# Kernel optimization log

Hardware: AMD Instinct MI355X
Metric: run time of the kernel (lower is better)

## Reference

```python
import jax, jax.numpy as jnp
import numpy as np

CHUNK = 128  # single steady-state chunk tier (T divisible by 128)
DECAY_MIN = 0.005


def setup_inputs() -> dict:
    key = jax.random.key(0)
    k0, k1, k2, k3, k4 = jax.random.split(key, 5)
    B, H, T, K = 4, 16, 2048, 64
    r = jax.random.normal(k0, (B, H, T, K), jnp.float32) * 0.5
    k = jax.random.normal(k1, (B, H, T, K), jnp.float32) * 0.5
    v = jax.random.normal(k2, (B, H, T, K), jnp.float32)
    # log-space decay (negative); mild magnitude keeps exp() of cumulative
    # in-chunk decays within fp32 range (torch original upcasts to fp64)
    w = -(jax.random.uniform(k3, (B, H, T, K), jnp.float32) * 0.2 + 0.01)
    u = jax.random.normal(k4, (1, H, 1, K), jnp.float32) * 0.5
    wkv_state = jnp.zeros((B, H, K, K), jnp.float32)
    return {"r": r, "k": k, "v": v, "w": w, "u": u, "wkv_state": wkv_state}


def _chunked_wkv(r, k, v, w, u, wkv_state):
    B, H, T, K = r.shape
    Tc = CHUNK
    N = T // Tc
    # decay preprocessing (log space)
    w_decay = jnp.clip(jnp.exp(w), DECAY_MIN, None)
    w_log = jnp.log(w_decay)
    wc = w_log.reshape(B, H, N, Tc, K)
    wc_cum = jnp.cumsum(wc, axis=-2)                       # inclusive cumsum
    shifted = jnp.pad(wc_cum[..., :-1, :], ((0, 0), (0, 0), (0, 0), (1, 0), (0, 0)))
    ws = wc.sum(axis=-2, keepdims=True)                    # (B,H,N,1,K)
    w_inter = jnp.exp(ws - wc_cum)                          # (B,H,N,Tc,K)
    w_intra = jnp.exp(wc_cum - wc)
    ws_e = jnp.exp(jnp.swapaxes(ws, -1, -2))               # (B,H,N,K,1)

    rc = r.reshape(B, H, N, Tc, K)
    kc = k.reshape(B, H, N, Tc, K)
    vc = v.reshape(B, H, N, Tc, K)

    # numerically-centered intra-chunk decays (offset at chunk midpoint)
    off = shifted[..., Tc // 2:Tc // 2 + 1, :]
    r_dec = jnp.exp(shifted - off)
    k_inv = jnp.exp(off - wc_cum)

    # intra-chunk attention: strictly-lower-triangular + u-bonus diagonal
    a = jnp.einsum('bhnik,bhnjk->bhnij', rc * r_dec, kc * k_inv)
    a = jnp.tril(a, -1)
    diag = jnp.einsum('bhntk,bhntk->bhnt', rc, u[:, :, None] * kc)
    a = a + diag[..., :, None] * jnp.eye(Tc, dtype=a.dtype)
    out = jnp.einsum('bhnij,bhnjv->bhniv', a, vc)

    # inter-chunk: sequential state carry via scan
    wkv = jnp.einsum('bhntk,bhntv->bhnkv', kc * w_inter, vc)   # (B,H,N,K,K)

    def step(state, inp):
        ws_i, wkv_i = inp
        return state * ws_i + wkv_i, state

    ws_s = jnp.moveaxis(ws_e, 2, 0)    # (N,B,H,K,1)
    wkv_s = jnp.moveaxis(wkv, 2, 0)    # (N,B,H,K,K)
    final_state, states = jax.lax.scan(step, wkv_state, (ws_s, wkv_s))
    states = jnp.moveaxis(states, 0, 2)  # (B,H,N,K,K) — state entering chunk n

    out = out + jnp.einsum('bhntk,bhnkv->bhntv', rc * w_intra, states)
    return out.reshape(B, H, T, K), final_state


def reference(r, k, v, w, u, wkv_state):
    return _chunked_wkv(r, k, v, w, u, wkv_state)
```

## Files before the change

### kernel.cpp

```cpp
#include <hip/hip_runtime.h>

#define TC 128
#define KD 64
#define WLOG_MIN (-5.2983174f)

typedef __attribute__((ext_vector_type(8))) short short8;
typedef __attribute__((ext_vector_type(4))) short short4_t;
typedef __attribute__((ext_vector_type(4))) float f32x4;

__device__ __forceinline__ unsigned short f2bf(float x) {
  union { float f; unsigned int u; } c; c.f = x;
  unsigned int u = c.u + 0x7fffu + ((c.u >> 16) & 1u);
  return (unsigned short)(u >> 16);
}
__device__ __forceinline__ float bf2f(unsigned short x) {
  union { unsigned int u; float f; } c; c.u = ((unsigned int)x) << 16; return c.f;
}


__global__ __launch_bounds__(512, 8)
void rwkv_wkv(const float* __restrict__ kk_, const float* __restrict__ vv,
              const float* __restrict__ ww,
              unsigned short* __restrict__ wkv_u16, float* __restrict__ wse_ws,
              int N) {
  __shared__ alignas(16) unsigned short vT_s[KD * TC];
  __shared__ alignas(16) unsigned short kiT_s[KD * TC];
  __shared__ alignas(16) float segtot[8 * 64];

  const int bid = blockIdx.x;
  const int n = bid % N, bh = bid / N;
  const size_t base = ((size_t)bh * N + n) * (TC * KD);
  const float *kg = kk_ + base, *vg = vv + base, *wg = ww + base;

  const int tid = threadIdx.x;
  const int lk = tid & 63;
  const int wv = tid >> 6;

  float wl[16];
  {
    float c = 0.f;
    #pragma unroll
    for (int tt = 0; tt < 16; ++tt) {
      wl[tt] = fmaxf(wg[(wv * 16 + tt) * KD + lk], WLOG_MIN);
      c += wl[tt];
    }
    segtot[wv * 64 + lk] = c;
  }
  __syncthreads();
  float segofs = 0.f, myoff = 0.f, wsum = 0.f;
  #pragma unroll
  for (int i = 0; i < 8; ++i) {
    const float si = segtot[i * 64 + lk];
    if (i < wv) segofs += si;
    if (i < 4) myoff += si;
    wsum += si;
  }
  const float wsoff_own = __expf(wsum - myoff);
  if (wv == 0) wse_ws[((size_t)bh * N + n) * KD + lk] = __expf(wsum);

  {
    float c = segofs;
    short8 vb8, kib8;
    #pragma unroll
    for (int tt = 0; tt < 16; ++tt) {
      const int t = wv * 16 + tt;
      const float kv = kg[t * KD + lk], vvv = vg[t * KD + lk];
      kib8[tt & 7] = (short)f2bf(kv * __expf(myoff - c - wl[tt]));
      vb8[tt & 7] = (short)f2bf(vvv);
      c += wl[tt];
      if ((tt & 7) == 7) {
        const int g = t >> 3;
        *(short8*)&vT_s[lk * TC + ((g ^ (lk & 7)) << 3)] = vb8;
        *(short8*)&kiT_s[lk * TC + ((g ^ (lk & 7)) << 3)] = kib8;
      }
    }
  }
  __syncthreads();

  {
    const int quad = lk >> 4, l16 = lk & 15;
    const int kt = wv >> 1;
    const int nb = (wv & 1) * 2;
    f32x4 acc[2] = {{0,0,0,0},{0,0,0,0}};
    const int row = kt * 16 + l16;
    #pragma unroll
    for (int ks = 0; ks < 4; ++ks) {
      short8 a = *(const short8*)&kiT_s[row * TC + (((ks * 4 + quad) ^ (row & 7)) << 3)];
      #pragma unroll
      for (int nn = 0; nn < 2; ++nn) {
        const int vd = (nb + nn) * 16 + l16;
        short8 b = *(const short8*)&vT_s[vd * TC + (((ks * 4 + quad) ^ (vd & 7)) << 3)];
        acc[nn] = __builtin_amdgcn_mfma_f32_16x16x32_bf16(a, b, acc[nn], 0, 0, 0);
      }
    }
    float wso[4];
    #pragma unroll
    for (int reg = 0; reg < 4; ++reg) wso[reg] = __shfl(wsoff_own, kt * 16 + quad * 4 + reg, 64);
    unsigned short* wkvg = wkv_u16 + ((size_t)bh * N + n) * (KD * KD);
    #pragma unroll
    for (int nn = 0; nn < 2; ++nn)
      #pragma unroll
      for (int reg = 0; reg < 4; ++reg)
        wkvg[(kt * 16 + quad * 4 + reg) * KD + (nb + nn) * 16 + l16] = f2bf(acc[nn][reg] * wso[reg]);
  }
}

__global__ __launch_bounds__(512, 4)
void rwkv_main(const float* __restrict__ rr, const float* __restrict__ kk_,
               const float* __restrict__ vv, const float* __restrict__ ww,
               const float* __restrict__ uu,
               const unsigned short* __restrict__ wkv_u16,
               const float* __restrict__ wse_ws,
               const float* __restrict__ st_in,
               float* __restrict__ out, float* __restrict__ final_out,
               int H, int N) {
  __shared__ alignas(16) unsigned short rd_s[TC * KD];
  __shared__ alignas(16) unsigned short ki_s[TC * KD];
  __shared__ alignas(16) unsigned short vT_s[KD * TC];
  __shared__ alignas(16) unsigned char su_raw[10240];
  __shared__ alignas(16) unsigned short diag_s[TC];
  float* segtot = (float*)su_raw;
  unsigned short* Ast = (unsigned short*)su_raw;

  const int bid = blockIdx.x;
  const int n = bid % N, bh = bid / N, h = bh % H;
  const size_t base = ((size_t)bh * N + n) * (TC * KD);
  const float *rg = rr + base, *kg = kk_ + base, *vg = vv + base, *wg = ww + base;

  const int tid = threadIdx.x;
  const int lk = tid & 63;
  const int wv = tid >> 6;
  const int quad = lk >> 4, l16 = lk & 15;
  const float uk = uu[h * KD + lk];

  float wl[16];
  {
    float c = 0.f;
    #pragma unroll
    for (int tt = 0; tt < 16; ++tt) {
      wl[tt] = fmaxf(wg[(wv * 16 + tt) * KD + lk], WLOG_MIN);
      c += wl[tt];
    }
    segtot[wv * 64 + lk] = c;
  }
  __syncthreads();
  float segofs = 0.f, myoff = 0.f;
  #pragma unroll
  for (int i = 0; i < 8; ++i) {
    const float si = segtot[i * 64 + lk];
    if (i < wv) segofs += si;
    if (i < 4) myoff += si;
  }
  const float eoff = __expf(myoff);

  unsigned int rwp[8];
  {
    float c = segofs;
    short8 vb8;
    float darr[8];
    #pragma unroll
    for (int tt = 0; tt < 16; ++tt) {
      const int t = wv * 16 + tt;
      const float rv = rg[t * KD + lk], kv = kg[t * KD + lk], vvv = vg[t * KD + lk];
      const int slot = (lk >> 3) ^ (t & 7) ^ ((t >> 3) & 7);
      const int nat = t * KD + (slot << 3) + (lk & 7);
      const float e1 = __expf(c - myoff);
      rd_s[nat] = f2bf(rv * e1);
      const unsigned short rwv = f2bf(rv * e1 * eoff);
      if (tt & 1) rwp[tt >> 1] |= ((unsigned int)rwv) << 16;
      else        rwp[tt >> 1]  = (unsigned int)rwv;
      ki_s[nat] = f2bf(kv * __expf(myoff - c - wl[tt]));
      vb8[tt & 7] = (short)f2bf(vvv);
      darr[tt & 7] = rv * uk * kv;
      c += wl[tt];
      if ((tt & 7) == 7) {
        const int g = t >> 3;
        *(short8*)&vT_s[lk * TC + ((g ^ (lk & 7)) << 3)] = vb8;
        #pragma unroll
        for (int o = 32; o > 0; o >>= 1)
          #pragma unroll
          for (int q = 0; q < 8; ++q) darr[q] += __shfl_xor(darr[q], o, 64);
        if (lk == 0) {
          short8 dpk;
          #pragma unroll
          for (int q = 0; q < 8; ++q) dpk[q] = (short)f2bf(darr[q]);
          *(short8*)&diag_s[g * 8] = dpk;
        }
      }
    }
  }
  __syncthreads();

  const int skd = tid >> 3, sv0 = (tid & 7) * 8;
  const size_t sbase = (size_t)bh * (KD * KD);
  float s[8];
  *(f32x4*)&s[0] = *(const f32x4*)&st_in[sbase + skd * KD + sv0];
  *(f32x4*)&s[4] = *(const f32x4*)&st_in[sbase + skd * KD + sv0 + 4];
  const float* wseb = wse_ws + (size_t)bh * N * KD + skd;
  const unsigned short* wkvb = wkv_u16 + (size_t)bh * N * (KD * KD) + skd * KD + sv0;
  {
    float e_c = 0.f; short8 x_c = {0};
    if (n > 0) {
      e_c = wseb[0];
      x_c = *(const short8*)&wkvb[0];
    }
    for (int j = 0; j < n; ++j) {
      const float e = e_c; const short8 x = x_c;
      if (j + 1 < n) {
        e_c = wseb[(size_t)(j + 1) * KD];
        x_c = *(const short8*)&wkvb[(size_t)(j + 1) * (KD * KD)];
      }
      #pragma unroll
      for (int i = 0; i < 8; ++i) s[i] = s[i] * e + bf2f((unsigned short)x[i]);
    }
  }

  f32x4 oacc[4];
  {
    const int ib = wv, i0 = ib * 16, irow = i0 + l16;
    const int rsw = (irow & 7) ^ ((irow >> 3) & 7);
    short8 b0 = *(const short8*)&rd_s[irow * KD + ((quad ^ rsw) << 3)];
    short8 b1 = *(const short8*)&rd_s[irow * KD + (((4 + quad) ^ rsw) << 3)];
    const float diag_i = bf2f(diag_s[irow]);
    #pragma unroll
    for (int nn = 0; nn < 4; ++nn) oacc[nn] = (f32x4){0, 0, 0, 0};
    const int npairs = (ib + 2) >> 1;
    unsigned short* astw = Ast + wv * 640;
    for (int jp = 0; jp < npairs; ++jp) {
      #pragma unroll
      for (int jj = 0; jj < 2; ++jj) {
        const int j = jp * 2 + jj;
        short4_t pk;
        if (j <= ib) {
          const int jrow = j * 16 + l16;
          const int jsw = (jrow & 7) ^ ((jrow >> 3) & 7);
          short8 a0 = *(const short8*)&ki_s[jrow * KD + ((quad ^ jsw) << 3)];
          short8 a1 = *(const short8*)&ki_s[jrow * KD + (((4 + quad) ^ jsw) << 3)];
          f32x4 at = {0, 0, 0, 0};
          at = __builtin_amdgcn_mfma_f32_16x16x32_bf16(a0, b0, at, 0, 0, 0);
          at = __builtin_amdgcn_mfma_f32_16x16x32_bf16(a1, b1, at, 0, 0, 0);
          #pragma unroll
          for (int reg = 0; reg < 4; ++reg) {
            const int je = j * 16 + quad * 4 + reg;
            float val = at[reg];
            if (j == ib) val = (je < irow) ? val : ((je == irow) ? diag_i : 0.f);
            pk[reg] = (short)f2bf(val);
          }
        } else {
          pk = (short4_t)0;
        }
        *(short4_t*)&astw[l16 * 40 + jj * 16 + quad * 4] = pk;
      }
      short8 af = *(const short8*)&astw[l16 * 40 + quad * 8];
      #pragma unroll
      for (int nn = 0; nn < 4; ++nn) {
        const int vd = nn * 16 + l16;
        short8 bv = *(const short8*)&vT_s[vd * TC + (((jp * 4 + quad) ^ (vd & 7)) << 3)];
        oacc[nn] = __builtin_amdgcn_mfma_f32_16x16x32_bf16(af, bv, oacc[nn], 0, 0, 0);
      }
    }
  }
  __syncthreads();

  {
    const int g = skd >> 3, k7 = skd & 7;
    #pragma unroll
    for (int i = 0; i < 8; ++i) {
      const int vd = sv0 + i;
      ki_s[vd * KD + (((g ^ (vd & 7)) << 3) | k7)] = f2bf(s[i]);
    }
  }
  #pragma unroll
  for (int tt = 0; tt < 16; ++tt) {
    const int t = wv * 16 + tt;
    const int slot = (lk >> 3) ^ (t & 7) ^ ((t >> 3) & 7);
    const int nat = t * KD + (slot << 3) + (lk & 7);
    const unsigned int pa = rwp[tt >> 1];
    rd_s[nat] = (unsigned short)((tt & 1) ? (pa >> 16) : (pa & 0xffffu));
  }
  if (n == N - 1) {
    const float e = wseb[(size_t)n * KD];
    const short8 x = *(const short8*)&wkvb[(size_t)n * (KD * KD)];
    #pragma unroll
    for (int i = 0; i < 8; ++i) s[i] = s[i] * e + bf2f((unsigned short)x[i]);
    *(f32x4*)&final_out[sbase + skd * KD + sv0] = *(const f32x4*)&s[0];
    *(f32x4*)&final_out[sbase + skd * KD + sv0 + 4] = *(const f32x4*)&s[4];
  }
  __syncthreads();

  {
    const int ib = wv, trow = ib * 16 + l16;
    const int rsw = (trow & 7) ^ ((trow >> 3) & 7);
    short8 a0 = *(const short8*)&rd_s[trow * KD + ((quad ^ rsw) << 3)];
    short8 a1 = *(const short8*)&rd_s[trow * KD + (((4 + quad) ^ rsw) << 3)];
    float* og = out + base;
    #pragma unroll
    for (int nn = 0; nn < 4; ++nn) {
      const int vd = nn * 16 + l16;
      short8 b0 = *(const short8*)&ki_s[vd * KD + ((quad ^ (vd & 7)) << 3)];
      short8 b1 = *(const short8*)&ki_s[vd * KD + (((4 + quad) ^ (vd & 7)) << 3)];
      f32x4 acc = {0, 0, 0, 0};
      acc = __builtin_amdgcn_mfma_f32_16x16x32_bf16(a0, b0, acc, 0, 0, 0);
      acc = __builtin_amdgcn_mfma_f32_16x16x32_bf16(a1, b1, acc, 0, 0, 0);
      #pragma unroll
      for (int reg = 0; reg < 4; ++reg)
        og[(size_t)(ib * 16 + quad * 4 + reg) * KD + nn * 16 + l16] = oacc[nn][reg] + acc[reg];
    }
  }
}

extern "C" void kernel_launch(void* const* d_in, const int* in_sizes, int n_in,
                              void* d_out, int out_size, void* d_ws, size_t ws_size,
                              hipStream_t stream) {
  const float* r = (const float*)d_in[0];
  const float* k = (const float*)d_in[1];
  const float* v = (const float*)d_in[2];
  const float* w = (const float*)d_in[3];
  const float* u = (const float*)d_in[4];
  const float* st0 = (const float*)d_in[5];
  float* out = (float*)d_out;

  const int BH = in_sizes[5] / (KD * KD);
  const int H = in_sizes[4] / KD;
  const int T = in_sizes[0] / (BH * KD);
  const int N = T / TC;

  unsigned short* wkv_u16 = (unsigned short*)d_ws;
  float* wse_ws = (float*)(wkv_u16 + (size_t)BH * N * KD * KD);
  float* final_out = out + (size_t)in_sizes[0];

  rwkv_wkv<<<BH * N, 512, 0, stream>>>(k, v, w, wkv_u16, wse_ws, N);
  rwkv_main<<<BH * N, 512, 0, stream>>>(r, k, v, w, u, wkv_u16, wse_ws, st0,
                                        out, final_out, H, N);
}
```

Measured before the change: 194.8 us.

## Vectorize chunk loads to float4 per lane and alias scratch LDS onto rd_s

Both kernels now load w, k, v (and r) as float4 per lane, with each lane covering 4 channels by 4 timesteps instead of 1 channel by 16 timesteps. The in-segment prefix sums are built with cross-lane shuffles and the LDS stores become short4 vector writes. The separate 10 KB su_raw scratch buffer is removed and its uses are aliased onto rd_s, which needs an extra barrier, and occupancy in rwkv_main is raised from 4 to 6 blocks. The goal is fewer, wider global memory transactions and lower LDS use for better occupancy, at the cost of more shuffles and possible register pressure under the tighter launch bound.

```diff
diff --git a/kernel.cpp b/kernel.cpp
--- a/kernel.cpp
+++ b/kernel.cpp
@@ -15,6 +15,12 @@
 }
 __device__ __forceinline__ float bf2f(unsigned short x) {
   union { unsigned int u; float f; } c; c.u = ((unsigned int)x) << 16; return c.f;
+}
+__device__ __forceinline__ f32x4 shfl4(f32x4 v, int src) {
+  f32x4 r;
+  #pragma unroll
+  for (int i = 0; i < 4; ++i) r[i] = __shfl(v[i], src, 64);
+  return r;
 }
 
 
@@ -33,52 +39,75 @@
   const float *kg = kk_ + base, *vg = vv + base, *wg = ww + base;
 
   const int tid = threadIdx.x;
-  const int lk = tid & 63;
-  const int wv = tid >> 6;
-
-  float wl[16];
-  {
-    float c = 0.f;
-    #pragma unroll
-    for (int tt = 0; tt < 16; ++tt) {
-      wl[tt] = fmaxf(wg[(wv * 16 + tt) * KD + lk], WLOG_MIN);
-      c += wl[tt];
-    }
-    segtot[wv * 64 + lk] = c;
-  }
-  __syncthreads();
-  float segofs = 0.f, myoff = 0.f, wsum = 0.f;
+  const int lane = tid & 63, wv = tid >> 6;
+  const int q = lane >> 4, c4 = lane & 15, kd0 = c4 * 4;
+
+  f32x4 wl4[4], k4[4], v4[4];
+  #pragma unroll
+  for (int j = 0; j < 4; ++j) {
+    const int t = wv * 16 + q * 4 + j;
+    wl4[j] = *(const f32x4*)&wg[t * KD + kd0];
+    k4[j] = *(const f32x4*)&kg[t * KD + kd0];
+    v4[j] = *(const f32x4*)&vg[t * KD + kd0];
+  }
+  #pragma unroll
+  for (int j = 0; j < 4; ++j)
+    #pragma unroll
+    for (int i = 0; i < 4; ++i) wl4[j][i] = fmaxf(wl4[j][i], WLOG_MIN);
+
+  const f32x4 ls = ((wl4[0] + wl4[1]) + wl4[2]) + wl4[3];
+  const f32x4 s0 = shfl4(ls, c4), s1 = shfl4(ls, 16 + c4);
+  const f32x4 s2 = shfl4(ls, 32 + c4), s3 = shfl4(ls, 48 + c4);
+  const f32x4 zero = {0.f, 0.f, 0.f, 0.f};
+  f32x4 pre = (q > 0 ? s0 : zero);
+  pre += (q > 1 ? s1 : zero);
+  pre += (q > 2 ? s2 : zero);
+  const f32x4 tot = ((s0 + s1) + s2) + s3;
+  if (q == 0) *(f32x4*)&segtot[wv * 64 + kd0] = tot;
+  __syncthreads();
+
+  f32x4 segofs4 = zero, myoff4 = zero, wsum4 = zero;
   #pragma unroll
   for (int i = 0; i < 8; ++i) {
-    const float si = segtot[i * 64 + lk];
-    if (i < wv) segofs += si;
-    if (i < 4) myoff += si;
-    wsum += si;
-  }
-  const float wsoff_own = __expf(wsum - myoff);
-  if (wv == 0) wse_ws[((size_t)bh * N + n) * KD + lk] = __expf(wsum);
-
-  {
-    float c = segofs;
-    short8 vb8, kib8;
-    #pragma unroll
-    for (int tt = 0; tt < 16; ++tt) {
-      const int t = wv * 16 + tt;
-      const float kv = kg[t * KD + lk], vvv = vg[t * KD + lk];
-      kib8[tt & 7] = (short)f2bf(kv * __expf(myoff - c - wl[tt]));
-      vb8[tt & 7] = (short)f2bf(vvv);
-      c += wl[tt];
-      if ((tt & 7) == 7) {
-        const int g = t >> 3;
-        *(short8*)&vT_s[lk * TC + ((g ^ (lk & 7)) << 3)] = vb8;
-        *(short8*)&kiT_s[lk * TC + ((g ^ (lk & 7)) << 3)] = kib8;
-      }
-    }
-  }
-  __syncthreads();
-
-  {
-    const int quad = lk >> 4, l16 = lk & 15;
+    const f32x4 si = *(const f32x4*)&segtot[i * 64 + kd0];
+    if (i < wv) segofs4 += si;
+    if (i < 4) myoff4 += si;
+    wsum4 += si;
+  }
+  f32x4 wsoff4;
+  #pragma unroll
+  for (int i = 0; i < 4; ++i) wsoff4[i] = __expf(wsum4[i] - myoff4[i]);
+  if (wv == 0 && q == 0) {
+    f32x4 e;
+    #pragma unroll
+    for (int i = 0; i < 4; ++i) e[i] = __expf(wsum4[i]);
+    *(f32x4*)&wse_ws[((size_t)bh * N + n) * KD + kd0] = e;
+  }
+
+  {
+    f32x4 cc = segofs4 + pre;
+    short4_t kib[4], vb[4];
+    #pragma unroll
+    for (int j = 0; j < 4; ++j) {
+      #pragma unroll
+      for (int i = 0; i < 4; ++i) {
+        kib[i][j] = (short)f2bf(k4[j][i] * __expf(myoff4[i] - cc[i] - wl4[j][i]));
+        vb[i][j] = (short)f2bf(v4[j][i]);
+      }
+      cc += wl4[j];
+    }
+    const int g = wv * 2 + (q >> 1), p4 = (q & 1) * 4;
+    #pragma unroll
+    for (int i = 0; i < 4; ++i) {
+      const int kd = kd0 + i;
+      *(short4_t*)&kiT_s[kd * TC + ((g ^ (kd & 7)) << 3) + p4] = kib[i];
+      *(short4_t*)&vT_s[kd * TC + ((g ^ (kd & 7)) << 3) + p4] = vb[i];
+    }
+  }
+  __syncthreads();
+
+  {
+    const int quad = lane >> 4, l16 = lane & 15;
     const int kt = wv >> 1;
     const int nb = (wv & 1) * 2;
     f32x4 acc[2] = {{0,0,0,0},{0,0,0,0}};
@@ -95,7 +124,7 @@
     }
     float wso[4];
     #pragma unroll
-    for (int reg = 0; reg < 4; ++reg) wso[reg] = __shfl(wsoff_own, kt * 16 + quad * 4 + reg, 64);
+    for (int reg = 0; reg < 4; ++reg) wso[reg] = __shfl(wsoff4[reg], kt * 4 + quad, 64);
     unsigned short* wkvg = wkv_u16 + ((size_t)bh * N + n) * (KD * KD);
     #pragma unroll
     for (int nn = 0; nn < 2; ++nn)
@@ -105,7 +134,7 @@
   }
 }
 
-__global__ __launch_bounds__(512, 4)
+__global__ __launch_bounds__(512, 6)
 void rwkv_main(const float* __restrict__ rr, const float* __restrict__ kk_,
                const float* __restrict__ vv, const float* __restrict__ ww,
                const float* __restrict__ uu,
@@ -117,10 +146,8 @@
   __shared__ alignas(16) unsigned short rd_s[TC * KD];
   __shared__ alignas(16) unsigned short ki_s[TC * KD];
   __shared__ alignas(16) unsigned short vT_s[KD * TC];
-  __shared__ alignas(16) unsigned char su_raw[10240];
   __shared__ alignas(16) unsigned short diag_s[TC];
-  float* segtot = (float*)su_raw;
-  unsigned short* Ast = (unsigned short*)su_raw;
+  float* segtot = (float*)rd_s;
 
   const int bid = blockIdx.x;
   const int n = bid % N, bh = bid / N, h = bh % H;
@@ -128,65 +155,88 @@
   const float *rg = rr + base, *kg = kk_ + base, *vg = vv + base, *wg = ww + base;
 
   const int tid = threadIdx.x;
-  const int lk = tid & 63;
-  const int wv = tid >> 6;
-  const int quad = lk >> 4, l16 = lk & 15;
-  const float uk = uu[h * KD + lk];
-
-  float wl[16];
-  {
-    float c = 0.f;
-    #pragma unroll
-    for (int tt = 0; tt < 16; ++tt) {
-      wl[tt] = fmaxf(wg[(wv * 16 + tt) * KD + lk], WLOG_MIN);
-      c += wl[tt];
-    }
-    segtot[wv * 64 + lk] = c;
-  }
-  __syncthreads();
-  float segofs = 0.f, myoff = 0.f;
+  const int lane = tid & 63, wv = tid >> 6;
+  const int q = lane >> 4, c4 = lane & 15, kd0 = c4 * 4;
+  const int quad = lane >> 4, l16 = lane & 15;
+  const f32x4 uk4 = *(const f32x4*)&uu[h * KD + kd0];
+
+  f32x4 wl4[4], r4[4], k4[4], v4[4];
+  #pragma unroll
+  for (int j = 0; j < 4; ++j) {
+    const int t = wv * 16 + q * 4 + j;
+    wl4[j] = *(const f32x4*)&wg[t * KD + kd0];
+    r4[j] = *(const f32x4*)&rg[t * KD + kd0];
+    k4[j] = *(const f32x4*)&kg[t * KD + kd0];
+    v4[j] = *(const f32x4*)&vg[t * KD + kd0];
+  }
+  #pragma unroll
+  for (int j = 0; j < 4; ++j)
+    #pragma unroll
+    for (int i = 0; i < 4; ++i) wl4[j][i] = fmaxf(wl4[j][i], WLOG_MIN);
+
+  const f32x4 ls = ((wl4[0] + wl4[1]) + wl4[2]) + wl4[3];
+  const f32x4 s0 = shfl4(ls, c4), s1 = shfl4(ls, 16 + c4);
+  const f32x4 s2 = shfl4(ls, 32 + c4), s3 = shfl4(ls, 48 + c4);
+  const f32x4 zero = {0.f, 0.f, 0.f, 0.f};
+  f32x4 pre = (q > 0 ? s0 : zero);
+  pre += (q > 1 ? s1 : zero);
+  pre += (q > 2 ? s2 : zero);
+  const f32x4 tot = ((s0 + s1) + s2) + s3;
+  if (q == 0) *(f32x4*)&segtot[wv * 64 + kd0] = tot;
+  __syncthreads();
+  f32x4 segofs4 = zero, myoff4 = zero;
   #pragma unroll
   for (int i = 0; i < 8; ++i) {
-    const float si = segtot[i * 64 + lk];
-    if (i < wv) segofs += si;
-    if (i < 4) myoff += si;
-  }
-  const float eoff = __expf(myoff);
-
-  unsigned int rwp[8];
-  {
-    float c = segofs;
-    short8 vb8;
-    float darr[8];
-    #pragma unroll
-    for (int tt = 0; tt < 16; ++tt) {
-      const int t = wv * 16 + tt;
-      const float rv = rg[t * KD + lk], kv = kg[t * KD + lk], vvv = vg[t * KD + lk];
-      const int slot = (lk >> 3) ^ (t & 7) ^ ((t >> 3) & 7);
-      const int nat = t * KD + (slot << 3) + (lk & 7);
-      const float e1 = __expf(c - myoff);
-      rd_s[nat] = f2bf(rv * e1);
-      const unsigned short rwv = f2bf(rv * e1 * eoff);
-      if (tt & 1) rwp[tt >> 1] |= ((unsigned int)rwv) << 16;
-      else        rwp[tt >> 1]  = (unsigned int)rwv;
-      ki_s[nat] = f2bf(kv * __expf(myoff - c - wl[tt]));
-      vb8[tt & 7] = (short)f2bf(vvv);
-      darr[tt & 7] = rv * uk * kv;
-      c += wl[tt];
-      if ((tt & 7) == 7) {
-        const int g = t >> 3;
-        *(short8*)&vT_s[lk * TC + ((g ^ (lk & 7)) << 3)] = vb8;
-        #pragma unroll
-        for (int o = 32; o > 0; o >>= 1)
-          #pragma unroll
-          for (int q = 0; q < 8; ++q) darr[q] += __shfl_xor(darr[q], o, 64);
-        if (lk == 0) {
-          short8 dpk;
-          #pragma unroll
-          for (int q = 0; q < 8; ++q) dpk[q] = (short)f2bf(darr[q]);
-          *(short8*)&diag_s[g * 8] = dpk;
-        }
-      }
+    const f32x4 si = *(const f32x4*)&segtot[i * 64 + kd0];
+    if (i < wv) segofs4 += si;
+    if (i < 4) myoff4 += si;
+  }
+  __syncthreads();
+  f32x4 eoff4;
+  #pragma unroll
+  for (int i = 0; i < 4; ++i) eoff4[i] = __expf(myoff4[i]);
+
+  short4_t rwq[4];
+  {
+    f32x4 cc = segofs4 + pre;
+    short4_t vb[4];
+    float dar[4];
+    #pragma unroll
+    for (int j = 0; j < 4; ++j) {
+      const int t = wv * 16 + q * 4 + j;
+      const int addr = t * KD + (((c4 >> 1) ^ (t & 7) ^ ((t >> 3) & 7)) << 3) + (c4 & 1) * 4;
+      short4_t rdv, kiv;
+      #pragma unroll
+      for (int i = 0; i < 4; ++i) {
+        const float e1 = __expf(cc[i] - myoff4[i]);
+        rdv[i] = (short)f2bf(r4[j][i] * e1);
+        rwq[j][i] = (short)f2bf(r4[j][i] * e1 * eoff4[i]);
+        kiv[i] = (short)f2bf(k4[j][i] * __expf(myoff4[i] - cc[i] - wl4[j][i]));
+        vb[i][j] = (short)f2bf(v4[j][i]);
+      }
+      *(short4_t*)&rd_s[addr] = rdv;
+      *(short4_t*)&ki_s[addr] = kiv;
+      dar[j] = r4[j][0] * uk4[0] * k4[j][0];
+      dar[j] += r4[j][1] * uk4[1] * k4[j][1];
+      dar[j] += r4[j][2] * uk4[2] * k4[j][2];
+      dar[j] += r4[j][3] * uk4[3] * k4[j][3];
+      cc += wl4[j];
+    }
+    const int g = wv * 2 + (q >> 1), p4 = (q & 1) * 4;
+    #pragma unroll
+    for (int i = 0; i < 4; ++i) {
+      const int kd = kd0 + i;
+      *(short4_t*)&vT_s[kd * TC + ((g ^ (kd & 7)) << 3) + p4] = vb[i];
+    }
+    #pragma unroll
+    for (int o = 8; o > 0; o >>= 1)
+      #pragma unroll
+      for (int j = 0; j < 4; ++j) dar[j] += __shfl_xor(dar[j], o, 64);
+    if (c4 == 0) {
+      short4_t dp;
+      #pragma unroll
+      for (int j = 0; j < 4; ++j) dp[j] = (short)f2bf(dar[j]);
+      *(short4_t*)&diag_s[wv * 16 + q * 4] = dp;
     }
   }
   __syncthreads();
@@ -225,7 +275,7 @@
     #pragma unroll
     for (int nn = 0; nn < 4; ++nn) oacc[nn] = (f32x4){0, 0, 0, 0};
     const int npairs = (ib + 2) >> 1;
-    unsigned short* astw = Ast + wv * 640;
+    unsigned short* astw = &rd_s[wv * 16 * KD];
     for (int jp = 0; jp < npairs; ++jp) {
       #pragma unroll
       for (int jj = 0; jj < 2; ++jj) {
@@ -271,12 +321,10 @@
     }
   }
   #pragma unroll
-  for (int tt = 0; tt < 16; ++tt) {
-    const int t = wv * 16 + tt;
-    const int slot = (lk >> 3) ^ (t & 7) ^ ((t >> 3) & 7);
-    const int nat = t * KD + (slot << 3) + (lk & 7);
-    const unsigned int pa = rwp[tt >> 1];
-    rd_s[nat] = (unsigned short)((tt & 1) ? (pa >> 16) : (pa & 0xffffu));
+  for (int j = 0; j < 4; ++j) {
+    const int t = wv * 16 + q * 4 + j;
+    const int addr = t * KD + (((c4 >> 1) ^ (t & 7) ^ ((t >> 3) & 7)) << 3) + (c4 & 1) * 4;
+    *(short4_t*)&rd_s[addr] = rwq[j];
   }
   if (n == N - 1) {
     const float e = wseb[(size_t)n * KD];
```

Measured after the change: 257.4 us. +32.1%, slower.
